# Performance work log

Hardware: AMD Instinct MI355X
Metric: run time of the kernel (lower is better)

Reference implementation:

```python
import jax, jax.numpy as jnp
import numpy as np
from jax import lax

B, H, W, C_IN, C_OUT = 32, 56, 56, 256, 256
KH, KW = 3, 3

def setup_inputs() -> dict:
    key = jax.random.key(0)
    k_in, k_kern, k_bias = jax.random.split(key, 3)
    inputs = jax.random.normal(k_in, (B, H, W, C_IN), dtype=jnp.float32)
    # lecun_normal (flax default_kernel_init): std = 1/sqrt(fan_in)
    fan_in = KH * KW * C_IN
    kernel = jax.random.normal(k_kern, (KH, KW, C_IN, C_OUT), dtype=jnp.float32) / jnp.sqrt(fan_in).astype(jnp.float32)
    bias = jnp.zeros((C_OUT,), dtype=jnp.float32)
    return {"inputs": inputs, "kernel": kernel, "bias": bias}

def reference(inputs, kernel, bias):
    # QuantConv forward with config noise == 0.0: plain NHWC/HWIO conv + bias.
    y = lax.conv_general_dilated(
        inputs, kernel,
        window_strides=(1, 1),
        padding='SAME',
        lhs_dilation=(1, 1),
        rhs_dilation=(1, 1),
        dimension_numbers=('NHWC', 'HWIO', 'NHWC'),
        feature_group_count=1,
    )
    return y + bias
```

## Files before the change

### kernel.cpp

```cpp
#include <hip/hip_runtime.h>
#include <hip/hip_bf16.h>
#include <stdint.h>


#define IMG_B 32
#define IMG_H 56
#define IMG_W 56
#define CIN   256
#define COUT  256
#define KDIM  2304
#define M_TOT 100352
#define HW    (IMG_H * IMG_W)
#define PW    58
#define PHW   (PW * PW)

typedef __bf16 bf16_t;
typedef bf16_t bf16x8 __attribute__((ext_vector_type(8)));
typedef float  f32x4  __attribute__((ext_vector_type(4)));

typedef const __attribute__((address_space(1))) void GV;
typedef __attribute__((address_space(3))) void LV;

__device__ __forceinline__ void async16(const bf16_t* g, bf16_t* l) {
    __builtin_amdgcn_global_load_lds((GV*)g, (LV*)l, 16, 0, 0);
}

__global__ void prep_pad(const float* __restrict__ in, bf16_t* __restrict__ out) {
    const size_t e = ((size_t)blockIdx.x * 256 + threadIdx.x) * 8;
    const int pix = (int)(e >> 8);
    const int c0  = (int)(e & 255);
    const int b   = pix / PHW;
    const int r   = pix - b * PHW;
    const int py  = r / PW;
    const int px  = r - py * PW;
    bf16x8 v = {};
    if (py >= 1 && py <= IMG_H && px >= 1 && px <= IMG_W) {
        const f32x4* s = (const f32x4*)(in +
            ((((size_t)b * IMG_H + (py - 1)) * IMG_W + (px - 1)) << 8) + c0);
        f32x4 a = s[0], bq = s[1];
        #pragma unroll
        for (int k = 0; k < 4; ++k) v[k] = (bf16_t)a[k];
        #pragma unroll
        for (int k = 0; k < 4; ++k) v[4 + k] = (bf16_t)bq[k];
    }
    *(bf16x8*)(out + e) = v;
}

__global__ void prep_weights(const float* __restrict__ kern, bf16_t* __restrict__ wt) {
    int idx = blockIdx.x * 256 + threadIdx.x;
    int co  = idx / KDIM;
    int k   = idx - co * KDIM;
    wt[idx] = (bf16_t)kern[k * COUT + co];
}

__global__ __launch_bounds__(256)
void conv_mfma_p(const bf16_t* __restrict__ P, const bf16_t* __restrict__ wt,
                 const float* __restrict__ bias, float* __restrict__ out)
{
    __shared__ bf16_t Al[128 * 32];
    __shared__ bf16_t Bl[128 * 32];

    const int tid  = threadIdx.x;
    const int wave = tid >> 6;
    const int lane = tid & 63;

    const int bid   = blockIdx.x;
    const int tile  = (bid & 7) * 196 + (bid >> 3);
    const int ntile = tile & 1;
    const int mtile = tile >> 1;

    const int rloc = lane >> 2;
    const int seg  = lane & 3;

    const bf16_t* abase[2];
    const bf16_t* wrow[2];
    bf16_t* alds[2];
    bf16_t* blds[2];
    #pragma unroll
    for (int j = 0; j < 2; ++j) {
        const int m   = mtile * 128 + j * 64 + wave * 16 + rloc;
        const int bb  = m / HW;
        const int rem = m - bb * HW;
        const int yy  = rem / IMG_W;
        const int xx  = rem - yy * IMG_W;
        abase[j] = P + (((size_t)bb * PHW + yy * PW + xx) << 8) + seg * 8;
        const int co = ntile * 128 + j * 64 + wave * 16 + rloc;
        wrow[j] = wt + (size_t)co * KDIM + seg * 8;
        alds[j] = &Al[(j * 64 + wave * 16) * 32];
        blds[j] = &Bl[(j * 64 + wave * 16) * 32];
    }

    const int wm   = wave & 1;
    const int wn   = wave >> 1;
    const int lrow = lane & 15;
    const int q    = lane >> 4;

    f32x4 acc[4][4] = {};

    #pragma unroll 1
    for (int it = 0; it < 72; ++it) {
        const int tap = it >> 3;
        const int kh  = tap / 3;
        const int kw  = tap - kh * 3;
        const int koff = ((kh * PW + kw) << 8) + ((it & 7) << 5);

        #pragma unroll
        for (int j = 0; j < 2; ++j) {
            async16(abase[j] + koff, alds[j]);
            async16(wrow[j] + it * 32, blds[j]);
        }

        __syncthreads();

        bf16x8 af[4], bf[4];
        #pragma unroll
        for (int i = 0; i < 4; ++i)
            af[i] = *(const bf16x8*)(&Al[(wm * 64 + i * 16 + lrow) * 32 + q * 8]);
        #pragma unroll
        for (int j = 0; j < 4; ++j)
            bf[j] = *(const bf16x8*)(&Bl[(wn * 64 + j * 16 + lrow) * 32 + q * 8]);

        #pragma unroll
        for (int i = 0; i < 4; ++i)
            #pragma unroll
            for (int j = 0; j < 4; ++j)
                acc[i][j] = __builtin_amdgcn_mfma_f32_16x16x32_bf16(af[i], bf[j], acc[i][j], 0, 0, 0);

        __syncthreads();
    }

    const int co_base = ntile * 128 + wn * 64;
    float bv[4];
    #pragma unroll
    for (int j = 0; j < 4; ++j) bv[j] = bias[co_base + j * 16 + lrow];

    const int mrow_base = mtile * 128 + wm * 64;
    #pragma unroll
    for (int i = 0; i < 4; ++i) {
        #pragma unroll
        for (int rr = 0; rr < 4; ++rr) {
            const int mm = mrow_base + i * 16 + q * 4 + rr;
            float* op = out + (size_t)mm * COUT + co_base;
            #pragma unroll
            for (int j = 0; j < 4; ++j)
                op[j * 16 + lrow] = acc[i][j][rr] + bv[j];
        }
    }
}

#define ASTR 40
#define BSTR 40
__global__ __launch_bounds__(256)
void conv_mfma(const float* __restrict__ in, const bf16_t* __restrict__ wt,
               const float* __restrict__ bias, float* __restrict__ out)
{
    __shared__ bf16_t Alf[128 * ASTR];
    __shared__ bf16_t Blf[128 * BSTR];

    const int tid   = threadIdx.x;
    const int ntile = blockIdx.x & 1;
    const int mtile = blockIdx.x >> 1;

    const int arow = tid >> 1;
    const int aseg = tid & 1;
    const int m    = mtile * 128 + arow;
    const int bb   = m / HW;
    const int rem  = m - bb * HW;
    const int yy   = rem / IMG_W;
    const int xx   = rem - yy * IMG_W;

    const bf16_t* wt_row = wt + (size_t)(ntile * 128 + arow) * KDIM + aseg * 16;

    const int wave = tid >> 6;
    const int lane = tid & 63;
    const int wm   = wave & 1;
    const int wn   = wave >> 1;
    const int lrow = lane & 15;
    const int q    = lane >> 4;

    f32x4 acc[4][4] = {};

    #pragma unroll 1
    for (int it = 0; it < 72; ++it) {
        const int tap = it >> 3;
        const int kh  = tap / 3;
        const int kw  = tap - kh * 3;
        const int ci0 = (it & 7) << 5;

        const int iy = yy + kh - 1;
        const int ix = xx + kw - 1;
        const bool valid = ((unsigned)iy < IMG_H) && ((unsigned)ix < IMG_W);

        f32x4 va[4] = {};
        if (valid) {
            const f32x4* src = (const f32x4*)(in +
                ((((size_t)bb * IMG_H + iy) * IMG_W + ix) * CIN + ci0 + aseg * 16));
            va[0] = src[0]; va[1] = src[1]; va[2] = src[2]; va[3] = src[3];
        }
        const uint4 wb0 = *(const uint4*)(wt_row + it * 32);
        const uint4 wb1 = *(const uint4*)(wt_row + it * 32 + 8);

        __syncthreads();

        bf16x8 pa0, pa1;
        #pragma unroll
        for (int e = 0; e < 8; ++e) pa0[e] = (bf16_t)va[e >> 2][e & 3];
        #pragma unroll
        for (int e = 0; e < 8; ++e) pa1[e] = (bf16_t)va[2 + (e >> 2)][e & 3];
        *(bf16x8*)(&Alf[arow * ASTR + aseg * 16])     = pa0;
        *(bf16x8*)(&Alf[arow * ASTR + aseg * 16 + 8]) = pa1;
        *(uint4*)(&Blf[arow * BSTR + aseg * 16])      = wb0;
        *(uint4*)(&Blf[arow * BSTR + aseg * 16 + 8])  = wb1;

        __syncthreads();

        bf16x8 af[4], bf[4];
        #pragma unroll
        for (int i = 0; i < 4; ++i)
            af[i] = *(const bf16x8*)(&Alf[(wm * 64 + i * 16 + lrow) * ASTR + q * 8]);
        #pragma unroll
        for (int j = 0; j < 4; ++j)
            bf[j] = *(const bf16x8*)(&Blf[(wn * 64 + j * 16 + lrow) * BSTR + q * 8]);

        #pragma unroll
        for (int i = 0; i < 4; ++i)
            #pragma unroll
            for (int j = 0; j < 4; ++j)
                acc[i][j] = __builtin_amdgcn_mfma_f32_16x16x32_bf16(af[i], bf[j], acc[i][j], 0, 0, 0);
    }

    const int co_base = ntile * 128 + wn * 64;
    float bv[4];
    #pragma unroll
    for (int j = 0; j < 4; ++j) bv[j] = bias[co_base + j * 16 + lrow];

    const int mrow_base = mtile * 128 + wm * 64;
    #pragma unroll
    for (int i = 0; i < 4; ++i) {
        #pragma unroll
        for (int rr = 0; rr < 4; ++rr) {
            const int mm = mrow_base + i * 16 + q * 4 + rr;
            float* op = out + (size_t)mm * COUT + co_base;
            #pragma unroll
            for (int j = 0; j < 4; ++j)
                op[j * 16 + lrow] = acc[i][j][rr] + bv[j];
        }
    }
}

extern "C" void kernel_launch(void* const* d_in, const int* in_sizes, int n_in,
                              void* d_out, int out_size, void* d_ws, size_t ws_size,
                              hipStream_t stream) {
    const float* inputs = (const float*)d_in[0];
    const float* kernel = (const float*)d_in[1];
    const float* bias   = (const float*)d_in[2];
    float*       outp   = (float*)d_out;

    const size_t p_elems = (size_t)IMG_B * PHW * CIN;
    const size_t p_bytes = p_elems * sizeof(bf16_t);
    const size_t w_bytes = (size_t)KDIM * COUT * sizeof(bf16_t);

    if (ws_size >= p_bytes + w_bytes) {
        bf16_t* pimg = (bf16_t*)d_ws;
        bf16_t* wt   = (bf16_t*)((char*)d_ws + p_bytes);
        prep_pad<<<(int)(p_elems / 8 / 256), 256, 0, stream>>>(inputs, pimg);
        prep_weights<<<KDIM * COUT / 256, 256, 0, stream>>>(kernel, wt);
        conv_mfma_p<<<(M_TOT / 128) * 2, 256, 0, stream>>>(pimg, wt, bias, outp);
    } else {
        bf16_t* wt = (bf16_t*)d_ws;
        prep_weights<<<KDIM * COUT / 256, 256, 0, stream>>>(kernel, wt);
        conv_mfma<<<(M_TOT / 128) * 2, 256, 0, stream>>>(inputs, wt, bias, outp);
    }
}
```

Before: 363.5 us.

## Use 32x32x16 MFMA with BK=64, XOR-swizzled LDS and register prefetch overlap

Reworks the implicit-GEMM conv kernel to use a K tile of 64 (36 iterations instead of 72), the 32x32x16 bf16 MFMA with 2x2 accumulator blocks per wave, and an XOR swizzle on the LDS layout to avoid bank conflicts. Fragments are loaded from LDS into registers first, and the next tile's async global-to-LDS loads are issued before the MFMAs run, so memory traffic overlaps compute. The aim is fewer barriers, fewer LDS reads per MFMA, and better latency hiding. In exchange it uses more LDS and more registers for the fragment arrays.

```diff
diff --git a/kernel.cpp b/kernel.cpp
--- a/kernel.cpp
+++ b/kernel.cpp
@@ -13,10 +13,13 @@
 #define HW    (IMG_H * IMG_W)
 #define PW    58
 #define PHW   (PW * PW)
+#define BK    64
+#define ITERS (KDIM / BK)
 
 typedef __bf16 bf16_t;
 typedef bf16_t bf16x8 __attribute__((ext_vector_type(8)));
 typedef float  f32x4  __attribute__((ext_vector_type(4)));
+typedef float  f32x16 __attribute__((ext_vector_type(16)));
 
 typedef const __attribute__((address_space(1))) void GV;
 typedef __attribute__((address_space(3))) void LV;
@@ -57,8 +60,8 @@
 void conv_mfma_p(const bf16_t* __restrict__ P, const bf16_t* __restrict__ wt,
                  const float* __restrict__ bias, float* __restrict__ out)
 {
-    __shared__ bf16_t Al[128 * 32];
-    __shared__ bf16_t Bl[128 * 32];
+    __shared__ bf16_t Al[128 * BK];
+    __shared__ bf16_t Bl[128 * BK];
 
     const int tid  = threadIdx.x;
     const int wave = tid >> 6;
@@ -69,81 +72,98 @@
     const int ntile = tile & 1;
     const int mtile = tile >> 1;
 
-    const int rloc = lane >> 2;
-    const int seg  = lane & 3;
-
-    const bf16_t* abase[2];
-    const bf16_t* wrow[2];
-    bf16_t* alds[2];
-    bf16_t* blds[2];
-    #pragma unroll
-    for (int j = 0; j < 2; ++j) {
-        const int m   = mtile * 128 + j * 64 + wave * 16 + rloc;
+    const int rl = lane >> 3;
+    const int sl = lane & 7;
+    const int u  = sl ^ rl;
+
+    const bf16_t* asrc[4];
+    const bf16_t* bsrc[4];
+    bf16_t* alds[4];
+    bf16_t* blds[4];
+    #pragma unroll
+    for (int i = 0; i < 4; ++i) {
+        const int row = wave * 32 + i * 8 + rl;
+        const int m   = mtile * 128 + row;
         const int bb  = m / HW;
         const int rem = m - bb * HW;
         const int yy  = rem / IMG_W;
         const int xx  = rem - yy * IMG_W;
-        abase[j] = P + (((size_t)bb * PHW + yy * PW + xx) << 8) + seg * 8;
-        const int co = ntile * 128 + j * 64 + wave * 16 + rloc;
-        wrow[j] = wt + (size_t)co * KDIM + seg * 8;
-        alds[j] = &Al[(j * 64 + wave * 16) * 32];
-        blds[j] = &Bl[(j * 64 + wave * 16) * 32];
-    }
-
-    const int wm   = wave & 1;
-    const int wn   = wave >> 1;
-    const int lrow = lane & 15;
-    const int q    = lane >> 4;
-
-    f32x4 acc[4][4] = {};
+        asrc[i] = P + (((size_t)bb * PHW + yy * PW + xx) << 8) + u * 8;
+        const int co = ntile * 128 + row;
+        bsrc[i] = wt + (size_t)co * KDIM + u * 8;
+        alds[i] = &Al[(wave * 32 + i * 8) * BK];
+        blds[i] = &Bl[(wave * 32 + i * 8) * BK];
+    }
+
+    const int wm = wave & 1;
+    const int wn = wave >> 1;
+    const int ln = lane & 31;
+    const int lh = lane >> 5;
+    const int rx = ln & 7;
+
+    f32x16 acc[2][2] = {};
+
+    #pragma unroll
+    for (int i = 0; i < 4; ++i) {
+        async16(asrc[i], alds[i]);
+        async16(bsrc[i], blds[i]);
+    }
 
     #pragma unroll 1
-    for (int it = 0; it < 72; ++it) {
-        const int tap = it >> 3;
-        const int kh  = tap / 3;
-        const int kw  = tap - kh * 3;
-        const int koff = ((kh * PW + kw) << 8) + ((it & 7) << 5);
-
-        #pragma unroll
-        for (int j = 0; j < 2; ++j) {
-            async16(abase[j] + koff, alds[j]);
-            async16(wrow[j] + it * 32, blds[j]);
-        }
-
-        __syncthreads();
-
-        bf16x8 af[4], bf[4];
-        #pragma unroll
-        for (int i = 0; i < 4; ++i)
-            af[i] = *(const bf16x8*)(&Al[(wm * 64 + i * 16 + lrow) * 32 + q * 8]);
-        #pragma unroll
-        for (int j = 0; j < 4; ++j)
-            bf[j] = *(const bf16x8*)(&Bl[(wn * 64 + j * 16 + lrow) * 32 + q * 8]);
-
-        #pragma unroll
-        for (int i = 0; i < 4; ++i)
-            #pragma unroll
-            for (int j = 0; j < 4; ++j)
-                acc[i][j] = __builtin_amdgcn_mfma_f32_16x16x32_bf16(af[i], bf[j], acc[i][j], 0, 0, 0);
-
-        __syncthreads();
-    }
-
-    const int co_base = ntile * 128 + wn * 64;
-    float bv[4];
-    #pragma unroll
-    for (int j = 0; j < 4; ++j) bv[j] = bias[co_base + j * 16 + lrow];
-
-    const int mrow_base = mtile * 128 + wm * 64;
-    #pragma unroll
-    for (int i = 0; i < 4; ++i) {
-        #pragma unroll
-        for (int rr = 0; rr < 4; ++rr) {
-            const int mm = mrow_base + i * 16 + q * 4 + rr;
-            float* op = out + (size_t)mm * COUT + co_base;
-            #pragma unroll
-            for (int j = 0; j < 4; ++j)
-                op[j * 16 + lrow] = acc[i][j][rr] + bv[j];
+    for (int it = 0; it < ITERS; ++it) {
+        __syncthreads();
+
+        bf16x8 af[2][4], bf[2][4];
+        #pragma unroll
+        for (int kk = 0; kk < 4; ++kk) {
+            const int slot = ((kk * 2 + lh) ^ rx) * 8;
+            #pragma unroll
+            for (int g = 0; g < 2; ++g) {
+                af[g][kk] = *(const bf16x8*)(&Al[(wm * 64 + g * 32 + ln) * BK + slot]);
+                bf[g][kk] = *(const bf16x8*)(&Bl[(wn * 64 + g * 32 + ln) * BK + slot]);
+            }
+        }
+
+        __syncthreads();
+
+        if (it + 1 < ITERS) {
+            const int itn  = it + 1;
+            const int tap  = itn >> 2;
+            const int kh   = tap / 3;
+            const int kw   = tap - kh * 3;
+            const int koff = ((kh * PW + kw) << 8) + ((itn & 3) << 6);
+            const int woff = itn * BK;
+            #pragma unroll
+            for (int i = 0; i < 4; ++i) {
+                async16(asrc[i] + koff, alds[i]);
+                async16(bsrc[i] + woff, blds[i]);
+            }
+        }
+
+        #pragma unroll
+        for (int kk = 0; kk < 4; ++kk)
+            #pragma unroll
+            for (int g = 0; g < 2; ++g)
+                #pragma unroll
+                for (int h = 0; h < 2; ++h)
+                    acc[g][h] = __builtin_amdgcn_mfma_f32_32x32x16_bf16(
+                        af[g][kk], bf[h][kk], acc[g][h], 0, 0, 0);
+    }
+
+    const int mbase  = mtile * 128 + wm * 64;
+    const int cobase = ntile * 128 + wn * 64;
+    float bv[2];
+    #pragma unroll
+    for (int h = 0; h < 2; ++h) bv[h] = bias[cobase + h * 32 + ln];
+
+    #pragma unroll
+    for (int g = 0; g < 2; ++g) {
+        #pragma unroll
+        for (int reg = 0; reg < 16; ++reg) {
+            const int mm = mbase + g * 32 + (reg & 3) + 8 * (reg >> 2) + 4 * lh;
+            float* op = out + (size_t)mm * COUT + cobase + ln;
+            op[0]  = acc[g][0][reg] + bv[0];
+            op[32] = acc[g][1][reg] + bv[1];
         }
     }
 }
```

Measured after the change: 315.1 us. 1.15x faster.
